# Optimization experiments

Hardware: AMD Instinct MI355X
Metric: run time of the kernel (lower is better)

## Reference

```python
import jax, jax.numpy as jnp
import numpy as np

SQRT2 = 1.4142135623730951

def _oyzx2spin():
    # 0yzx -> (uu, ud, du, dd) spin projection matrix, complex64
    M = np.array([[1, 0, 1, 0],
                  [0, -1j, 0, 1],
                  [0, 1j, 0, 1],
                  [1, 0, -1, 0]], dtype=np.complex64) / SQRT2
    return jnp.asarray(M)


def setup_inputs() -> dict:
    key = jax.random.key(0)
    B, C_real, nL, nR = 65536, 8, 13, 13  # C_real = 2 * C_complex (soc_complex_doubling), C_complex % 4 == 0
    HR_in = jax.random.normal(key, (B, C_real, nL, nR), dtype=jnp.float32)
    return {"HR_in": HR_in}


def reference(HR_in):
    # Faithful translation of E3Hamiltonian._spin_projection with
    # real storage + soc_complex_doubling=True.
    B, C_real, nL, nR = HR_in.shape
    half = C_real // 2  # complex channel count
    # pack complex-doubled real storage into complex channels
    HR_c = jax.lax.complex(HR_in[:, :half], HR_in[:, half:])  # [B, half, nL, nR] complex
    n_chunks = half // 4
    HR_view = HR_c.reshape(B, n_chunks, 4, nL, nR)  # 4 = (0, y, z, x) spin components
    M = _oyzx2spin()  # [4(spin), 4(0yzx)]
    # project 0yzx components onto (uu, ud, du, dd) spin basis
    HR_proj = jnp.einsum('nkslr,ps->nkplr', HR_view, M)
    HR_proj_flat = HR_proj.reshape(B, half, nL, nR)
    # unpack back to real storage: [real-half | imag-half] along channel dim
    return jnp.concatenate([HR_proj_flat.real, HR_proj_flat.imag], axis=1)
```

## Files before the change

kernel.cpp:

```cpp
#include <hip/hip_runtime.h>


#define PLANE 169
#define CSTRIDE 1352
#define QUADS 338
#define WAVES 4

__global__ __launch_bounds__(256) void spin_proj_kernel(
    const float4* __restrict__ in, float4* __restrict__ out) {
    __shared__ float lds[WAVES * CSTRIDE];

    const int wave = threadIdx.x >> 6;
    const int lane = threadIdx.x & 63;
    float* slab = lds + wave * CSTRIDE;
    float4* slab4 = (float4*)slab;

    const size_t item = (size_t)blockIdx.x * WAVES + wave;
    const float4* __restrict__ gin = in + item * QUADS;
    float4* __restrict__ gout = out + item * QUADS;

    #pragma unroll
    for (int k = 0; k < 6; ++k) {
        int v = lane + k * 64;
        if (v < QUADS) slab4[v] = gin[v];
    }
    asm volatile("s_waitcnt lgkmcnt(0)" ::: "memory");
    __builtin_amdgcn_wave_barrier();

    const float sc = 0.70710678118654752440f;
    #pragma unroll
    for (int k = 0; k < 3; ++k) {
        int j = lane + k * 64;
        if (j < PLANE) {
            float r0 = slab[0 * PLANE + j];
            float r1 = slab[1 * PLANE + j];
            float r2 = slab[2 * PLANE + j];
            float r3 = slab[3 * PLANE + j];
            float i0 = slab[4 * PLANE + j];
            float i1 = slab[5 * PLANE + j];
            float i2 = slab[6 * PLANE + j];
            float i3 = slab[7 * PLANE + j];
            slab[0 * PLANE + j] = (r0 + r2) * sc;
            slab[1 * PLANE + j] = (i1 + r3) * sc;
            slab[2 * PLANE + j] = (r3 - i1) * sc;
            slab[3 * PLANE + j] = (r0 - r2) * sc;
            slab[4 * PLANE + j] = (i0 + i2) * sc;
            slab[5 * PLANE + j] = (i3 - r1) * sc;
            slab[6 * PLANE + j] = (r1 + i3) * sc;
            slab[7 * PLANE + j] = (i0 - i2) * sc;
        }
    }
    asm volatile("s_waitcnt lgkmcnt(0)" ::: "memory");
    __builtin_amdgcn_wave_barrier();

    #pragma unroll
    for (int k = 0; k < 6; ++k) {
        int v = lane + k * 64;
        if (v < QUADS) gout[v] = slab4[v];
    }
}

extern "C" void kernel_launch(void* const* d_in, const int* in_sizes, int n_in,
                              void* d_out, int out_size, void* d_ws, size_t ws_size,
                              hipStream_t stream) {
    const float4* in = (const float4*)d_in[0];
    float4* out = (float4*)d_out;

    int n_items = in_sizes[0] / CSTRIDE;
    int grid = n_items / WAVES;
    spin_proj_kernel<<<grid, 256, 0, stream>>>(in, out);
}
```

Before: 134.6 us.

## Use persistent grid-stride waves with register prefetch of the next item

Replaces the one-block-per-four-items launch with a fixed grid of 1792 blocks, where each wave loops over items with a stride. Inside the loop, the next item's global loads are issued into registers before the LDS transform and store of the current item, so load latency overlaps with compute and writes. This cuts block launch overhead but lowers the number of independent waves in flight, and it holds more live registers.

```diff
diff --git a/kernel.cpp b/kernel.cpp
--- a/kernel.cpp
+++ b/kernel.cpp
@@ -5,58 +5,78 @@
 #define CSTRIDE 1352
 #define QUADS 338
 #define WAVES 4
+#define BLOCKS 1792
 
 __global__ __launch_bounds__(256) void spin_proj_kernel(
-    const float4* __restrict__ in, float4* __restrict__ out) {
+    const float4* __restrict__ in, float4* __restrict__ out,
+    int n_items, int W) {
     __shared__ float lds[WAVES * CSTRIDE];
-
     const int wave = threadIdx.x >> 6;
     const int lane = threadIdx.x & 63;
     float* slab = lds + wave * CSTRIDE;
     float4* slab4 = (float4*)slab;
 
-    const size_t item = (size_t)blockIdx.x * WAVES + wave;
-    const float4* __restrict__ gin = in + item * QUADS;
-    float4* __restrict__ gout = out + item * QUADS;
+    const int v0 = lane,        v1 = lane + 64,  v2 = lane + 128;
+    const int v3 = lane + 192,  v4 = lane + 256, v5 = lane + 320;
+    const bool has5 = (v5 < QUADS);
 
-    #pragma unroll
-    for (int k = 0; k < 6; ++k) {
-        int v = lane + k * 64;
-        if (v < QUADS) slab4[v] = gin[v];
+    int it = blockIdx.x * WAVES + wave;
+    if (it >= n_items) return;
+
+    float4 p0, p1, p2, p3, p4, p5;
+    {
+        const float4* __restrict__ g = in + (size_t)it * QUADS;
+        p0 = g[v0]; p1 = g[v1]; p2 = g[v2]; p3 = g[v3]; p4 = g[v4];
+        if (has5) p5 = g[v5];
     }
-    asm volatile("s_waitcnt lgkmcnt(0)" ::: "memory");
-    __builtin_amdgcn_wave_barrier();
 
     const float sc = 0.70710678118654752440f;
-    #pragma unroll
-    for (int k = 0; k < 3; ++k) {
-        int j = lane + k * 64;
-        if (j < PLANE) {
-            float r0 = slab[0 * PLANE + j];
-            float r1 = slab[1 * PLANE + j];
-            float r2 = slab[2 * PLANE + j];
-            float r3 = slab[3 * PLANE + j];
-            float i0 = slab[4 * PLANE + j];
-            float i1 = slab[5 * PLANE + j];
-            float i2 = slab[6 * PLANE + j];
-            float i3 = slab[7 * PLANE + j];
-            slab[0 * PLANE + j] = (r0 + r2) * sc;
-            slab[1 * PLANE + j] = (i1 + r3) * sc;
-            slab[2 * PLANE + j] = (r3 - i1) * sc;
-            slab[3 * PLANE + j] = (r0 - r2) * sc;
-            slab[4 * PLANE + j] = (i0 + i2) * sc;
-            slab[5 * PLANE + j] = (i3 - r1) * sc;
-            slab[6 * PLANE + j] = (r1 + i3) * sc;
-            slab[7 * PLANE + j] = (i0 - i2) * sc;
+
+    while (it < n_items) {
+        slab4[v0] = p0; slab4[v1] = p1; slab4[v2] = p2;
+        slab4[v3] = p3; slab4[v4] = p4;
+        if (has5) slab4[v5] = p5;
+
+        const int nx = it + W;
+        if (nx < n_items) {
+            const float4* __restrict__ g = in + (size_t)nx * QUADS;
+            p0 = g[v0]; p1 = g[v1]; p2 = g[v2]; p3 = g[v3]; p4 = g[v4];
+            if (has5) p5 = g[v5];
         }
-    }
-    asm volatile("s_waitcnt lgkmcnt(0)" ::: "memory");
-    __builtin_amdgcn_wave_barrier();
 
-    #pragma unroll
-    for (int k = 0; k < 6; ++k) {
-        int v = lane + k * 64;
-        if (v < QUADS) gout[v] = slab4[v];
+        asm volatile("s_waitcnt lgkmcnt(0)" ::: "memory");
+        __builtin_amdgcn_wave_barrier();
+
+        #pragma unroll
+        for (int k = 0; k < 3; ++k) {
+            const int j = lane + k * 64;
+            if (k < 2 || j < PLANE) {
+                float r0 = slab[0*PLANE + j], r1 = slab[1*PLANE + j];
+                float r2 = slab[2*PLANE + j], r3 = slab[3*PLANE + j];
+                float i0 = slab[4*PLANE + j], i1 = slab[5*PLANE + j];
+                float i2 = slab[6*PLANE + j], i3 = slab[7*PLANE + j];
+                slab[0*PLANE + j] = (r0 + r2) * sc;
+                slab[1*PLANE + j] = (i1 + r3) * sc;
+                slab[2*PLANE + j] = (r3 - i1) * sc;
+                slab[3*PLANE + j] = (r0 - r2) * sc;
+                slab[4*PLANE + j] = (i0 + i2) * sc;
+                slab[5*PLANE + j] = (i3 - r1) * sc;
+                slab[6*PLANE + j] = (r1 + i3) * sc;
+                slab[7*PLANE + j] = (i0 - i2) * sc;
+            }
+        }
+
+        asm volatile("s_waitcnt lgkmcnt(0)" ::: "memory");
+        __builtin_amdgcn_wave_barrier();
+
+        {
+            float4* __restrict__ g = out + (size_t)it * QUADS;
+            g[v0] = slab4[v0]; g[v1] = slab4[v1]; g[v2] = slab4[v2];
+            g[v3] = slab4[v3]; g[v4] = slab4[v4];
+            if (has5) g[v5] = slab4[v5];
+        }
+
+        it = nx;
     }
 }
 
@@ -66,7 +86,11 @@
     const float4* in = (const float4*)d_in[0];
     float4* out = (float4*)d_out;
 
-    int n_items = in_sizes[0] / CSTRIDE;
-    int grid = n_items / WAVES;
-    spin_proj_kernel<<<grid, 256, 0, stream>>>(in, out);
+    const int n_items = in_sizes[0] / CSTRIDE;
+    int grid = BLOCKS;
+    int max_grid = (n_items + WAVES - 1) / WAVES;
+    if (grid > max_grid) grid = max_grid;
+    const int W = grid * WAVES;
+
+    spin_proj_kernel<<<grid, 256, 0, stream>>>(in, out, n_items, W);
 }
```

New measurement: 141.2 us. +4.9%, slower.

## Load input directly to LDS and compute outputs straight from LDS to global

Applied to the files above, without the earlier changes.

Global-to-register-to-LDS staging is replaced with global_load_lds direct DMA into shared memory. The separate in-place LDS transform and write-back pass is dropped. Each lane now computes its four output floats from two LDS reads per element, using bit-packed per-channel source indices and signed coefficients, and writes a float4 straight to global. This removes one LDS write/read round trip and a barrier, at the cost of scalar LDS gathers, integer division and a per-element branch across plane boundaries.

```diff
diff --git a/kernel.cpp b/kernel.cpp
--- a/kernel.cpp
+++ b/kernel.cpp
@@ -4,59 +4,68 @@
 #define PLANE 169
 #define CSTRIDE 1352
 #define QUADS 338
+#define TAIL 18
 #define WAVES 4
+
+typedef __attribute__((address_space(1))) const void g_as1;
+typedef __attribute__((address_space(3))) void l_as3;
+
+__device__ __forceinline__ void gload16(const void* gp, void* lp) {
+    g_as1* g = (g_as1*)(uintptr_t)gp;
+    l_as3* l = (l_as3*)(uint32_t)(uintptr_t)lp;
+    __builtin_amdgcn_global_load_lds(g, l, 16, 0, 0);
+}
 
 __global__ __launch_bounds__(256) void spin_proj_kernel(
     const float4* __restrict__ in, float4* __restrict__ out) {
     __shared__ float lds[WAVES * CSTRIDE];
-
     const int wave = threadIdx.x >> 6;
     const int lane = threadIdx.x & 63;
     float* slab = lds + wave * CSTRIDE;
     float4* slab4 = (float4*)slab;
 
     const size_t item = (size_t)blockIdx.x * WAVES + wave;
-    const float4* __restrict__ gin = in + item * QUADS;
+
+    {
+        const float4* __restrict__ g = in + item * QUADS;
+        #pragma unroll
+        for (int k = 0; k < 5; ++k)
+            gload16(g + k * 64 + lane, slab4 + k * 64);
+        if (lane < TAIL)
+            gload16(g + 320 + lane, slab4 + 320);
+    }
+    asm volatile("s_waitcnt vmcnt(0)" ::: "memory");
+    __builtin_amdgcn_sched_barrier(0);
+    __builtin_amdgcn_wave_barrier();
+
     float4* __restrict__ gout = out + item * QUADS;
-
     #pragma unroll
     for (int k = 0; k < 6; ++k) {
-        int v = lane + k * 64;
-        if (v < QUADS) slab4[v] = gin[v];
-    }
-    asm volatile("s_waitcnt lgkmcnt(0)" ::: "memory");
-    __builtin_amdgcn_wave_barrier();
+        const int q = lane + k * 64;
+        if (k == 5 && lane >= TAIL) break;
+        const int idx0 = 4 * q;
+        const int c0 = idx0 / PLANE;
+        const int j0 = idx0 - c0 * PLANE;
 
-    const float sc = 0.70710678118654752440f;
-    #pragma unroll
-    for (int k = 0; k < 3; ++k) {
-        int j = lane + k * 64;
-        if (j < PLANE) {
-            float r0 = slab[0 * PLANE + j];
-            float r1 = slab[1 * PLANE + j];
-            float r2 = slab[2 * PLANE + j];
-            float r3 = slab[3 * PLANE + j];
-            float i0 = slab[4 * PLANE + j];
-            float i1 = slab[5 * PLANE + j];
-            float i2 = slab[6 * PLANE + j];
-            float i3 = slab[7 * PLANE + j];
-            slab[0 * PLANE + j] = (r0 + r2) * sc;
-            slab[1 * PLANE + j] = (i1 + r3) * sc;
-            slab[2 * PLANE + j] = (r3 - i1) * sc;
-            slab[3 * PLANE + j] = (r0 - r2) * sc;
-            slab[4 * PLANE + j] = (i0 + i2) * sc;
-            slab[5 * PLANE + j] = (i3 - r1) * sc;
-            slab[6 * PLANE + j] = (r1 + i3) * sc;
-            slab[7 * PLANE + j] = (i0 - i2) * sc;
+        float4 o;
+        #pragma unroll
+        for (int e = 0; e < 4; ++e) {
+            int c = c0, j = j0 + e;
+            if (j >= PLANE) { c = c0 + 1; j -= PLANE; }
+            const int A = (0x41140330u >> (c * 4)) & 0xF;
+            const int Bc = (0x67762552u >> (c * 4)) & 0xF;
+            const unsigned ca_bits = 0x3F3504F3u | (((0x20u >> c) & 1u) << 31);
+            const unsigned cb_bits = 0x3F3504F3u | (((0x8Cu >> c) & 1u) << 31);
+            const float x = slab[A * PLANE + j];
+            const float y = slab[Bc * PLANE + j];
+            const float ca = __builtin_bit_cast(float, ca_bits);
+            const float cb = __builtin_bit_cast(float, cb_bits);
+            float v = x * ca;
+            v = fmaf(y, cb, v);
+            if (e == 0) o.x = v; else if (e == 1) o.y = v;
+            else if (e == 2) o.z = v; else o.w = v;
         }
-    }
-    asm volatile("s_waitcnt lgkmcnt(0)" ::: "memory");
-    __builtin_amdgcn_wave_barrier();
-
-    #pragma unroll
-    for (int k = 0; k < 6; ++k) {
-        int v = lane + k * 64;
-        if (v < QUADS) gout[v] = slab4[v];
+        gout[q] = o;
     }
 }
 
@@ -66,7 +75,7 @@
     const float4* in = (const float4*)d_in[0];
     float4* out = (float4*)d_out;
 
-    int n_items = in_sizes[0] / CSTRIDE;
-    int grid = n_items / WAVES;
+    const int n_items = in_sizes[0] / CSTRIDE;
+    const int grid = n_items / WAVES;
     spin_proj_kernel<<<grid, 256, 0, stream>>>(in, out);
 }
```

After: 131.3 us. 2.5% less time.
